# Kernel optimization log

Hardware: AMD Instinct MI355X
Metric: run time of the kernel (lower is better)

## Reference

```python
import jax, jax.numpy as jnp
import numpy as np

N = 40000      # nodes
E = 640000     # edges (avg degree 16)
F = 128        # num_features
D = 128        # embedding_size
G = 128        # graphs in batch


def _glorot(key, shape):
    fan_in = shape[-1]
    return jax.random.normal(key, shape, jnp.float32) / np.float32(np.sqrt(fan_in))


def setup_inputs() -> dict:
    key = jax.random.key(0)
    ks = jax.random.split(key, 20)
    inp = {
        "x": jax.random.normal(ks[0], (N, F), jnp.float32),
        "edge_index": jax.random.randint(ks[1], (2, E), 0, N, dtype=jnp.int32),
        "batch_index": jnp.sort(jax.random.randint(ks[2], (N,), 0, G, dtype=jnp.int32)),
    }
    dims = [(D, F), (D, D), (D, D), (D, D)]
    for i, (dout, din) in enumerate(dims):
        inp[f"Wroot{i}"] = _glorot(ks[3 + 3 * i], (dout, din))
        inp[f"Wrel{i}"] = _glorot(ks[4 + 3 * i], (dout, din))
        inp[f"b{i}"] = jnp.zeros((dout,), jnp.float32)
    inp["Wout"] = _glorot(ks[18], (1, D))
    inp["bout"] = jnp.zeros((1,), jnp.float32)
    return inp


def _graph_conv(h, src, dst, Wroot, Wrel, b, num_nodes):
    # PyG GraphConv (aggr='add'): out_i = W_root x_i + W_rel * sum_{j->i} x_j + b
    # Linear commutes with the sum, so aggregate first then one dense GEMM.
    agg = jax.ops.segment_sum(h[src], dst, num_segments=num_nodes)  # [N, din]
    return h @ Wroot.T + agg @ Wrel.T + b


def reference(x, edge_index, batch_index,
              Wroot0, Wrel0, b0, Wroot1, Wrel1, b1,
              Wroot2, Wrel2, b2, Wroot3, Wrel3, b3,
              Wout, bout):
    src, dst = edge_index[0], edge_index[1]
    n = x.shape[0]
    h = x.astype(jnp.float32)
    layers = [(Wroot0, Wrel0, b0), (Wroot1, Wrel1, b1),
              (Wroot2, Wrel2, b2), (Wroot3, Wrel3, b3)]
    for Wr, Wn, b in layers:
        h = jax.nn.gelu(_graph_conv(h, src, dst, Wr, Wn, b, n), approximate=False)
        # dropout p=0.5 -> identity at eval time
    # global mean pool over graphs (gap)
    sums = jax.ops.segment_sum(h, batch_index, num_segments=G)        # [G, D]
    counts = jax.ops.segment_sum(jnp.ones((n,), jnp.float32), batch_index, num_segments=G)
    pooled = sums / jnp.maximum(counts, 1.0)[:, None]
    return pooled @ Wout.T + bout  # [G, 1]
```

## Files before the change

kernel.cpp:

```cpp
#include <hip/hip_runtime.h>
#include <hip/hip_bf16.h>

typedef __bf16 bf16x8 __attribute__((ext_vector_type(8)));
typedef float  f32x4  __attribute__((ext_vector_type(4)));

__device__ __forceinline__ float blo(unsigned v) { return __uint_as_float(v << 16); }
__device__ __forceinline__ float bhi(unsigned v) { return __uint_as_float(v & 0xffff0000u); }
__device__ __forceinline__ unsigned short f2bf(float f) {
    unsigned u = __float_as_uint(f);
    u += 0x7fffu + ((u >> 16) & 1u);
    return (unsigned short)(u >> 16);
}
__device__ __forceinline__ float gelu_f(float x) {
    float t = 0.7978845608028654f * (x + 0.044715f * x * x * x);
    float e = __expf(2.0f * t);
    float th = 1.0f - 2.0f / (1.0f + e);
    return 0.5f * x * (1.0f + th);
}


__global__ void degree_kernel(const int* __restrict__ dst, int* __restrict__ deg, int E) {
    int e = blockIdx.x * blockDim.x + threadIdx.x;
    if (e < E) atomicAdd(&deg[dst[e]], 1);
}

__global__ void chunk_sum_kernel(const int* __restrict__ deg, int* __restrict__ bsum, int n) {
    int i = blockIdx.x * 1024 + threadIdx.x;
    int v = (i < n) ? deg[i] : 0;
#pragma unroll
    for (int m = 1; m < 64; m <<= 1) v += __shfl_xor(v, m, 64);
    __shared__ int ws[16];
    int wave = threadIdx.x >> 6, lane = threadIdx.x & 63;
    if (lane == 0) ws[wave] = v;
    __syncthreads();
    if (threadIdx.x == 0) {
        int s = 0;
#pragma unroll
        for (int k = 0; k < 16; ++k) s += ws[k];
        bsum[blockIdx.x] = s;
    }
}

__global__ void chunk_scan_kernel(const int* __restrict__ bsum, int* __restrict__ bbase,
                                  int nb, int* __restrict__ offsets, int n, int E) {
    int lane = threadIdx.x;
    int v = (lane < nb) ? bsum[lane] : 0;
    int s = v;
#pragma unroll
    for (int m = 1; m < 64; m <<= 1) {
        int t = __shfl_up(s, m, 64);
        if (lane >= m) s += t;
    }
    if (lane < nb) bbase[lane] = s - v;
    if (lane == 0) offsets[n] = E;
}

__global__ void scan_apply_kernel(const int* __restrict__ deg, const int* __restrict__ bbase,
                                  int* __restrict__ offsets, int* __restrict__ cursor, int n) {
    int i = blockIdx.x * 1024 + threadIdx.x;
    int lane = threadIdx.x & 63, wave = threadIdx.x >> 6;
    int v = (i < n) ? deg[i] : 0;
    int s = v;
#pragma unroll
    for (int m = 1; m < 64; m <<= 1) {
        int t = __shfl_up(s, m, 64);
        if (lane >= m) s += t;
    }
    __shared__ int ws[16];
    if (lane == 63) ws[wave] = s;
    __syncthreads();
    if (wave == 0 && lane < 16) {
        int wv = ws[lane];
        int ss = wv;
#pragma unroll
        for (int m = 1; m < 16; m <<= 1) {
            int t = __shfl_up(ss, m, 64);
            if (lane >= m) ss += t;
        }
        ws[lane] = ss - wv;
    }
    __syncthreads();
    int excl = (s - v) + ws[wave] + bbase[blockIdx.x];
    if (i < n) { offsets[i] = excl; cursor[i] = excl; }
}

__global__ void scatter_kernel(const int* __restrict__ src, const int* __restrict__ dst,
                               int* __restrict__ cursor, int* __restrict__ sorted_src, int E) {
    int e = blockIdx.x * blockDim.x + threadIdx.x;
    if (e < E) {
        int d = dst[e];
        int pos = atomicAdd(&cursor[d], 1);
        sorted_src[pos] = src[e];
    }
}

__global__ void bounds_kernel(const int* __restrict__ batch, int* __restrict__ gstart,
                              int N, int G) {
    int g = blockIdx.x * blockDim.x + threadIdx.x;
    if (g <= G) {
        int lo = 0, hi = N;
        while (lo < hi) {
            int mid = (lo + hi) >> 1;
            if (batch[mid] < g) lo = mid + 1; else hi = mid;
        }
        gstart[g] = lo;
    }
}

__global__ void cvt_kernel(const float4* __restrict__ in, ushort4* __restrict__ out, int n4) {
    int i = blockIdx.x * blockDim.x + threadIdx.x;
    if (i < n4) {
        float4 f = in[i];
        ushort4 o; o.x = f2bf(f.x); o.y = f2bf(f.y); o.z = f2bf(f.z); o.w = f2bf(f.w);
        out[i] = o;
    }
}

__global__ void build_wcat_all(const float* __restrict__ Wr0, const float* __restrict__ Wn0,
                               const float* __restrict__ Wr1, const float* __restrict__ Wn1,
                               const float* __restrict__ Wr2, const float* __restrict__ Wn2,
                               const float* __restrict__ Wr3, const float* __restrict__ Wn3,
                               __hip_bfloat16* __restrict__ wcat) {
    int idx = blockIdx.x * blockDim.x + threadIdx.x;
    if (idx >= 4 * 128 * 256) return;
    int l = idx >> 15;
    int j = (idx >> 8) & 127, k = idx & 255;
    const float* Wr = (l == 0) ? Wr0 : (l == 1) ? Wr1 : (l == 2) ? Wr2 : Wr3;
    const float* Wn = (l == 0) ? Wn0 : (l == 1) ? Wn1 : (l == 2) ? Wn2 : Wn3;
    float v = (k < 128) ? Wr[j * 128 + k] : Wn[j * 128 + (k - 128)];
    wcat[idx] = __float2bfloat16(v);
}

#define LDS_STRIDE 264
__global__ __launch_bounds__(512, 4)
void layer_kernel(const __hip_bfloat16* __restrict__ h,
                  const int* __restrict__ offsets,
                  const int* __restrict__ sorted_src,
                  const __hip_bfloat16* __restrict__ Wcat,
                  const float* __restrict__ bias,
                  __hip_bfloat16* __restrict__ out, int N) {
    __shared__ char lds[64 * LDS_STRIDE];
    int wave = threadIdx.x >> 6;
    int lane = threadIdx.x & 63;
    int row0 = blockIdx.x * 64;
    int half = lane >> 5, fl = lane & 31;
    const uint2* hu = (const uint2*)h;

#pragma unroll 1
    for (int i = 0; i < 8; ++i) {
        int lr = wave * 8 + i;
        int node = row0 + lr;
        if (node < N) {
            int s = offsets[node], e = offsets[node + 1];
            f32x4 A0 = {0,0,0,0}, A1 = {0,0,0,0}, A2 = {0,0,0,0}, A3 = {0,0,0,0};
            int t = s;
            for (; t + 8 <= e; t += 8) {
                int j0 = sorted_src[t + half];
                int j1 = sorted_src[t + 2 + half];
                int j2 = sorted_src[t + 4 + half];
                int j3 = sorted_src[t + 6 + half];
                uint2 v0 = hu[(size_t)j0 * 32 + fl];
                uint2 v1 = hu[(size_t)j1 * 32 + fl];
                uint2 v2 = hu[(size_t)j2 * 32 + fl];
                uint2 v3 = hu[(size_t)j3 * 32 + fl];
                A0[0] += blo(v0.x); A0[1] += bhi(v0.x); A0[2] += blo(v0.y); A0[3] += bhi(v0.y);
                A1[0] += blo(v1.x); A1[1] += bhi(v1.x); A1[2] += blo(v1.y); A1[3] += bhi(v1.y);
                A2[0] += blo(v2.x); A2[1] += bhi(v2.x); A2[2] += blo(v2.y); A2[3] += bhi(v2.y);
                A3[0] += blo(v3.x); A3[1] += bhi(v3.x); A3[2] += blo(v3.y); A3[3] += bhi(v3.y);
            }
            if (t + 4 <= e) {
                int j0 = sorted_src[t + half];
                int j1 = sorted_src[t + 2 + half];
                uint2 v0 = hu[(size_t)j0 * 32 + fl];
                uint2 v1 = hu[(size_t)j1 * 32 + fl];
                A0[0] += blo(v0.x); A0[1] += bhi(v0.x); A0[2] += blo(v0.y); A0[3] += bhi(v0.y);
                A1[0] += blo(v1.x); A1[1] += bhi(v1.x); A1[2] += blo(v1.y); A1[3] += bhi(v1.y);
                t += 4;
            }
            if (t + 2 <= e) {
                int j0 = sorted_src[t + half];
                uint2 v0 = hu[(size_t)j0 * 32 + fl];
                A0[0] += blo(v0.x); A0[1] += bhi(v0.x); A0[2] += blo(v0.y); A0[3] += bhi(v0.y);
                t += 2;
            }
            if (t < e && half == 0) {
                int j = sorted_src[t];
                uint2 v = hu[(size_t)j * 32 + fl];
                A1[0] += blo(v.x); A1[1] += bhi(v.x); A1[2] += blo(v.y); A1[3] += bhi(v.y);
            }
            float q0 = (A0[0] + A1[0]) + (A2[0] + A3[0]); q0 += __shfl_xor(q0, 32, 64);
            float q1 = (A0[1] + A1[1]) + (A2[1] + A3[1]); q1 += __shfl_xor(q1, 32, 64);
            float q2 = (A0[2] + A1[2]) + (A2[2] + A3[2]); q2 += __shfl_xor(q2, 32, 64);
            float q3 = (A0[3] + A1[3]) + (A2[3] + A3[3]); q3 += __shfl_xor(q3, 32, 64);
            if (half == 0) {
                ushort4 o; o.x = f2bf(q0); o.y = f2bf(q1); o.z = f2bf(q2); o.w = f2bf(q3);
                *reinterpret_cast<ushort4*>(&lds[lr * LDS_STRIDE + fl * 8]) = o;
            }
        }
    }
    __syncthreads();

    int la  = lane & 15;
    int keg = lane >> 4;
    int ke0 = keg * 8;
    int col = wave * 16 + la;

    bf16x8 b[8];
#pragma unroll
    for (int ks = 0; ks < 8; ++ks)
        b[ks] = *reinterpret_cast<const bf16x8*>(&Wcat[(size_t)col * 256 + ks * 32 + ke0]);
    float bv = bias[col];

    f32x4 acc[4];
#pragma unroll
    for (int m = 0; m < 4; ++m) {
        int r = row0 + m * 16 + la;
        if (r >= N) r = N - 1;
        const __hip_bfloat16* hr = &h[(size_t)r * 128];
        bf16x8 a[8];
#pragma unroll
        for (int ks = 0; ks < 4; ++ks)
            a[ks] = *reinterpret_cast<const bf16x8*>(&hr[ks * 32 + ke0]);
#pragma unroll
        for (int ks = 0; ks < 4; ++ks)
            a[ks + 4] = *reinterpret_cast<const bf16x8*>(
                &lds[(m * 16 + la) * LDS_STRIDE + ks * 64 + keg * 16]);
        f32x4 c = {0, 0, 0, 0};
#pragma unroll
        for (int ks = 0; ks < 8; ++ks)
            c = __builtin_amdgcn_mfma_f32_16x16x32_bf16(a[ks], b[ks], c, 0, 0, 0);
        acc[m] = c;
    }

    int r0 = row0 + (lane >> 4) * 4;
#pragma unroll
    for (int m = 0; m < 4; ++m) {
#pragma unroll
        for (int j = 0; j < 4; ++j) {
            int r = r0 + m * 16 + j;
            if (r < N)
                out[(size_t)r * 128 + col] = __float2bfloat16(gelu_f(acc[m][j] + bv));
        }
    }
}


__global__ void pool_partial(const __hip_bfloat16* __restrict__ h,
                             const int* __restrict__ batch,
                             const float* __restrict__ Wout,
                             float* __restrict__ outsum, int N) {
    int wid = blockIdx.x * 4 + (threadIdx.x >> 6);
    int lane = threadIdx.x & 63;
    int i0 = wid * 16;
    if (i0 >= N) return;
    int half = lane >> 5, fl = lane & 31;
    const uint2* hu = (const uint2*)h;
    float w0 = Wout[4 * fl], w1 = Wout[4 * fl + 1];
    float w2 = Wout[4 * fl + 2], w3 = Wout[4 * fl + 3];
    float dot = 0.f;
    int cur = -1;
#pragma unroll
    for (int t = 0; t < 8; ++t) {
        int i = i0 + 2 * t + half;
        if (i < N) {
            int g = batch[i];
            uint2 v = hu[(size_t)i * 32 + fl];
            float d = blo(v.x) * w0 + bhi(v.x) * w1 + blo(v.y) * w2 + bhi(v.y) * w3;
            if (g != cur) {
                if (cur >= 0) {
                    float r = dot;
#pragma unroll
                    for (int m = 16; m >= 1; m >>= 1) r += __shfl_xor(r, m, 64);
                    if (fl == 0) atomicAdd(&outsum[cur], r);
                }
                cur = g; dot = d;
            } else {
                dot += d;
            }
        }
    }
    if (cur >= 0) {
        float r = dot;
#pragma unroll
        for (int m = 16; m >= 1; m >>= 1) r += __shfl_xor(r, m, 64);
        if (fl == 0) atomicAdd(&outsum[cur], r);
    }
}

__global__ void pool_finish(const float* __restrict__ outsum,
                            const int* __restrict__ gstart,
                            const float* __restrict__ bout,
                            float* __restrict__ out, int G) {
    int g = blockIdx.x * blockDim.x + threadIdx.x;
    if (g < G) {
        float cnt = (float)(gstart[g + 1] - gstart[g]);
        out[g] = outsum[g] / fmaxf(cnt, 1.0f) + bout[0];
    }
}


extern "C" void kernel_launch(void* const* d_in, const int* in_sizes, int n_in,
                              void* d_out, int out_size, void* d_ws, size_t ws_size,
                              hipStream_t stream) {
    const float* x          = (const float*)d_in[0];
    const int*   edge_index = (const int*)d_in[1];
    const int*   batch      = (const int*)d_in[2];
    const float* Wroot[4] = {(const float*)d_in[3], (const float*)d_in[6],
                             (const float*)d_in[9], (const float*)d_in[12]};
    const float* Wrel[4]  = {(const float*)d_in[4], (const float*)d_in[7],
                             (const float*)d_in[10], (const float*)d_in[13]};
    const float* bias[4]  = {(const float*)d_in[5], (const float*)d_in[8],
                             (const float*)d_in[11], (const float*)d_in[14]};
    const float* Wout = (const float*)d_in[15];
    const float* bout = (const float*)d_in[16];
    float* out = (float*)d_out;

    const int N = in_sizes[2];
    const int E = in_sizes[1] / 2;
    const int G = 128;
    const int* src = edge_index;
    const int* dst = edge_index + E;

    char* ws = (char*)d_ws;
    size_t o = 0;
    auto alloc = [&](size_t bytes) { void* p = ws + o; o += (bytes + 255) & ~(size_t)255; return p; };

    __hip_bfloat16* hx   = (__hip_bfloat16*)alloc((size_t)N * 128 * 2);
    __hip_bfloat16* hb0  = (__hip_bfloat16*)alloc((size_t)N * 128 * 2);
    __hip_bfloat16* hb1  = (__hip_bfloat16*)alloc((size_t)N * 128 * 2);
    __hip_bfloat16* wcat = (__hip_bfloat16*)alloc((size_t)4 * 128 * 256 * 2);
    int* deg     = (int*)alloc((size_t)N * 4);
    int* offsets = (int*)alloc((size_t)(N + 1) * 4);
    int* cursor  = (int*)alloc((size_t)N * 4);
    int* sorted  = (int*)alloc((size_t)E * 4);
    int* gstart  = (int*)alloc((size_t)(G + 1) * 4);
    int* bsum    = (int*)alloc(64 * 4);
    int* bbase   = (int*)alloc(64 * 4);
    float* outsum = (float*)alloc((size_t)G * 4);

    const int nb = (N + 1023) / 1024;

    hipMemsetAsync(deg, 0, (size_t)N * 4, stream);
    degree_kernel<<<(E + 255) / 256, 256, 0, stream>>>(dst, deg, E);
    chunk_sum_kernel<<<nb, 1024, 0, stream>>>(deg, bsum, N);
    chunk_scan_kernel<<<1, 64, 0, stream>>>(bsum, bbase, nb, offsets, N, E);
    scan_apply_kernel<<<nb, 1024, 0, stream>>>(deg, bbase, offsets, cursor, N);
    scatter_kernel<<<(E + 255) / 256, 256, 0, stream>>>(src, dst, cursor, sorted, E);
    bounds_kernel<<<1, 256, 0, stream>>>(batch, gstart, N, G);

    cvt_kernel<<<(N * 128 / 4 + 255) / 256, 256, 0, stream>>>(
        (const float4*)x, (ushort4*)hx, N * 128 / 4);
    build_wcat_all<<<(4 * 128 * 256 + 255) / 256, 256, 0, stream>>>(
        Wroot[0], Wrel[0], Wroot[1], Wrel[1], Wroot[2], Wrel[2], Wroot[3], Wrel[3], wcat);

    __hip_bfloat16* hin = hx;
    __hip_bfloat16* houts[4] = {hb0, hb1, hb0, hb1};
    for (int l = 0; l < 4; ++l) {
        layer_kernel<<<(N + 63) / 64, 512, 0, stream>>>(
            hin, offsets, sorted, wcat + (size_t)l * 128 * 256, bias[l], houts[l], N);
        hin = houts[l];
    }

    hipMemsetAsync(outsum, 0, (size_t)G * 4, stream);
    pool_partial<<<((N + 15) / 16 + 3) / 4, 256, 0, stream>>>(hin, batch, Wout, outsum, N);
    pool_finish<<<1, 128, 0, stream>>>(outsum, gstart, bout, out, G);
}
```

Baseline: 399.4 us.

## Merge small setup and pooling kernels to cut launch count

```diff
diff --git a/kernel.cpp b/kernel.cpp
--- a/kernel.cpp
+++ b/kernel.cpp
@@ -19,9 +19,25 @@
 }
 
 
-__global__ void degree_kernel(const int* __restrict__ dst, int* __restrict__ deg, int E) {
+__global__ void degree_bounds_kernel(const int* __restrict__ dst, int* __restrict__ deg, int E,
+                                     const int* __restrict__ batch, int* __restrict__ gstart,
+                                     int N, int G, float* __restrict__ outsum,
+                                     int* __restrict__ done) {
     int e = blockIdx.x * blockDim.x + threadIdx.x;
     if (e < E) atomicAdd(&deg[dst[e]], 1);
+    if (blockIdx.x == 0) {
+        int t = threadIdx.x;
+        if (t <= G) {
+            int lo = 0, hi = N;
+            while (lo < hi) {
+                int mid = (lo + hi) >> 1;
+                if (batch[mid] < t) lo = mid + 1; else hi = mid;
+            }
+            gstart[t] = lo;
+        }
+        if (t < G) outsum[t] = 0.f;
+        if (t == 255) *done = 0;
+    }
 }
 
 __global__ void chunk_sum_kernel(const int* __restrict__ deg, int* __restrict__ bsum, int n) {
@@ -41,32 +57,31 @@
     }
 }
 
-__global__ void chunk_scan_kernel(const int* __restrict__ bsum, int* __restrict__ bbase,
-                                  int nb, int* __restrict__ offsets, int n, int E) {
-    int lane = threadIdx.x;
-    int v = (lane < nb) ? bsum[lane] : 0;
+__global__ void scan_apply_kernel(const int* __restrict__ deg, const int* __restrict__ bsum,
+                                  int nb, int* __restrict__ offsets, int* __restrict__ cursor,
+                                  int n, int E) {
+    __shared__ int base_s;
+    __shared__ int ws[16];
+    int lane = threadIdx.x & 63, wave = threadIdx.x >> 6;
+    if (wave == 0) {
+        int v = (lane < nb) ? bsum[lane] : 0;
+        int s = v;
+#pragma unroll
+        for (int m = 1; m < 64; m <<= 1) {
+            int t = __shfl_up(s, m, 64);
+            if (lane >= m) s += t;
+        }
+        if (lane == (int)blockIdx.x) base_s = s - v;
+    }
+    __syncthreads();
+    int i = blockIdx.x * 1024 + threadIdx.x;
+    int v = (i < n) ? deg[i] : 0;
     int s = v;
 #pragma unroll
     for (int m = 1; m < 64; m <<= 1) {
         int t = __shfl_up(s, m, 64);
         if (lane >= m) s += t;
     }
-    if (lane < nb) bbase[lane] = s - v;
-    if (lane == 0) offsets[n] = E;
-}
-
-__global__ void scan_apply_kernel(const int* __restrict__ deg, const int* __restrict__ bbase,
-                                  int* __restrict__ offsets, int* __restrict__ cursor, int n) {
-    int i = blockIdx.x * 1024 + threadIdx.x;
-    int lane = threadIdx.x & 63, wave = threadIdx.x >> 6;
-    int v = (i < n) ? deg[i] : 0;
-    int s = v;
-#pragma unroll
-    for (int m = 1; m < 64; m <<= 1) {
-        int t = __shfl_up(s, m, 64);
-        if (lane >= m) s += t;
-    }
-    __shared__ int ws[16];
     if (lane == 63) ws[wave] = s;
     __syncthreads();
     if (wave == 0 && lane < 16) {
@@ -80,8 +95,9 @@
         ws[lane] = ss - wv;
     }
     __syncthreads();
-    int excl = (s - v) + ws[wave] + bbase[blockIdx.x];
+    int excl = (s - v) + ws[wave] + base_s;
     if (i < n) { offsets[i] = excl; cursor[i] = excl; }
+    if (blockIdx.x == 0 && threadIdx.x == 0) offsets[n] = E;
 }
 
 __global__ void scatter_kernel(const int* __restrict__ src, const int* __restrict__ dst,
@@ -94,41 +110,26 @@
     }
 }
 
-__global__ void bounds_kernel(const int* __restrict__ batch, int* __restrict__ gstart,
-                              int N, int G) {
-    int g = blockIdx.x * blockDim.x + threadIdx.x;
-    if (g <= G) {
-        int lo = 0, hi = N;
-        while (lo < hi) {
-            int mid = (lo + hi) >> 1;
-            if (batch[mid] < g) lo = mid + 1; else hi = mid;
-        }
-        gstart[g] = lo;
-    }
-}
-
-__global__ void cvt_kernel(const float4* __restrict__ in, ushort4* __restrict__ out, int n4) {
+__global__ void prep_kernel(const float4* __restrict__ x4, ushort4* __restrict__ hx4, int n4,
+                            const float* __restrict__ Wr0, const float* __restrict__ Wn0,
+                            const float* __restrict__ Wr1, const float* __restrict__ Wn1,
+                            const float* __restrict__ Wr2, const float* __restrict__ Wn2,
+                            const float* __restrict__ Wr3, const float* __restrict__ Wn3,
+                            __hip_bfloat16* __restrict__ wcat) {
     int i = blockIdx.x * blockDim.x + threadIdx.x;
     if (i < n4) {
-        float4 f = in[i];
+        float4 f = x4[i];
         ushort4 o; o.x = f2bf(f.x); o.y = f2bf(f.y); o.z = f2bf(f.z); o.w = f2bf(f.w);
-        out[i] = o;
-    }
-}
-
-__global__ void build_wcat_all(const float* __restrict__ Wr0, const float* __restrict__ Wn0,
-                               const float* __restrict__ Wr1, const float* __restrict__ Wn1,
-                               const float* __restrict__ Wr2, const float* __restrict__ Wn2,
-                               const float* __restrict__ Wr3, const float* __restrict__ Wn3,
-                               __hip_bfloat16* __restrict__ wcat) {
-    int idx = blockIdx.x * blockDim.x + threadIdx.x;
-    if (idx >= 4 * 128 * 256) return;
-    int l = idx >> 15;
-    int j = (idx >> 8) & 127, k = idx & 255;
-    const float* Wr = (l == 0) ? Wr0 : (l == 1) ? Wr1 : (l == 2) ? Wr2 : Wr3;
-    const float* Wn = (l == 0) ? Wn0 : (l == 1) ? Wn1 : (l == 2) ? Wn2 : Wn3;
-    float v = (k < 128) ? Wr[j * 128 + k] : Wn[j * 128 + (k - 128)];
-    wcat[idx] = __float2bfloat16(v);
+        hx4[i] = o;
+    }
+    if (i < 4 * 128 * 256) {
+        int l = i >> 15;
+        int j = (i >> 8) & 127, k = i & 255;
+        const float* Wr = (l == 0) ? Wr0 : (l == 1) ? Wr1 : (l == 2) ? Wr2 : Wr3;
+        const float* Wn = (l == 0) ? Wn0 : (l == 1) ? Wn1 : (l == 2) ? Wn2 : Wn3;
+        float v = (k < 128) ? Wr[j * 128 + k] : Wn[j * 128 + (k - 128)];
+        wcat[i] = __float2bfloat16(v);
+    }
 }
 
 #define LDS_STRIDE 264
@@ -245,56 +246,62 @@
 }
 
 
-__global__ void pool_partial(const __hip_bfloat16* __restrict__ h,
-                             const int* __restrict__ batch,
-                             const float* __restrict__ Wout,
-                             float* __restrict__ outsum, int N) {
+__global__ void pool_kernel(const __hip_bfloat16* __restrict__ h,
+                            const int* __restrict__ batch,
+                            const float* __restrict__ Wout,
+                            const int* __restrict__ gstart,
+                            const float* __restrict__ bout,
+                            float* __restrict__ outsum, int* __restrict__ done,
+                            float* __restrict__ out, int N, int G, int nblocks) {
     int wid = blockIdx.x * 4 + (threadIdx.x >> 6);
     int lane = threadIdx.x & 63;
     int i0 = wid * 16;
-    if (i0 >= N) return;
     int half = lane >> 5, fl = lane & 31;
-    const uint2* hu = (const uint2*)h;
-    float w0 = Wout[4 * fl], w1 = Wout[4 * fl + 1];
-    float w2 = Wout[4 * fl + 2], w3 = Wout[4 * fl + 3];
-    float dot = 0.f;
-    int cur = -1;
-#pragma unroll
-    for (int t = 0; t < 8; ++t) {
-        int i = i0 + 2 * t + half;
-        if (i < N) {
-            int g = batch[i];
-            uint2 v = hu[(size_t)i * 32 + fl];
-            float d = blo(v.x) * w0 + bhi(v.x) * w1 + blo(v.y) * w2 + bhi(v.y) * w3;
-            if (g != cur) {
-                if (cur >= 0) {
-                    float r = dot;
-#pragma unroll
-                    for (int m = 16; m >= 1; m >>= 1) r += __shfl_xor(r, m, 64);
-                    if (fl == 0) atomicAdd(&outsum[cur], r);
+    if (i0 < N) {
+        const uint2* hu = (const uint2*)h;
+        float w0 = Wout[4 * fl], w1 = Wout[4 * fl + 1];
+        float w2 = Wout[4 * fl + 2], w3 = Wout[4 * fl + 3];
+        float dot = 0.f;
+        int cur = -1;
+#pragma unroll
+        for (int t = 0; t < 8; ++t) {
+            int i = i0 + 2 * t + half;
+            if (i < N) {
+                int g = batch[i];
+                uint2 v = hu[(size_t)i * 32 + fl];
+                float d = blo(v.x) * w0 + bhi(v.x) * w1 + blo(v.y) * w2 + bhi(v.y) * w3;
+                if (g != cur) {
+                    if (cur >= 0) {
+                        float r = dot;
+#pragma unroll
+                        for (int m = 16; m >= 1; m >>= 1) r += __shfl_xor(r, m, 64);
+                        if (fl == 0) atomicAdd(&outsum[cur], r);
+                    }
+                    cur = g; dot = d;
+                } else {
+                    dot += d;
                 }
-                cur = g; dot = d;
-            } else {
-                dot += d;
-            }
-        }
-    }
-    if (cur >= 0) {
-        float r = dot;
-#pragma unroll
-        for (int m = 16; m >= 1; m >>= 1) r += __shfl_xor(r, m, 64);
-        if (fl == 0) atomicAdd(&outsum[cur], r);
-    }
-}
-
-__global__ void pool_finish(const float* __restrict__ outsum,
-                            const int* __restrict__ gstart,
-                            const float* __restrict__ bout,
-                            float* __restrict__ out, int G) {
-    int g = blockIdx.x * blockDim.x + threadIdx.x;
-    if (g < G) {
-        float cnt = (float)(gstart[g + 1] - gstart[g]);
-        out[g] = outsum[g] / fmaxf(cnt, 1.0f) + bout[0];
+            }
+        }
+        if (cur >= 0) {
+            float r = dot;
+#pragma unroll
+            for (int m = 16; m >= 1; m >>= 1) r += __shfl_xor(r, m, 64);
+            if (fl == 0) atomicAdd(&outsum[cur], r);
+        }
+    }
+    __threadfence();
+    __syncthreads();
+    __shared__ int is_last;
+    if (threadIdx.x == 0) is_last = (atomicAdd(done, 1) == nblocks - 1);
+    __syncthreads();
+    if (is_last) {
+        __threadfence();
+        int t = threadIdx.x;
+        if (t < G) {
+            float cnt = (float)(gstart[t + 1] - gstart[t]);
+            out[t] = outsum[t] / fmaxf(cnt, 1.0f) + bout[0];
+        }
     }
 }
 
@@ -335,22 +342,20 @@
     int* sorted  = (int*)alloc((size_t)E * 4);
     int* gstart  = (int*)alloc((size_t)(G + 1) * 4);
     int* bsum    = (int*)alloc(64 * 4);
-    int* bbase   = (int*)alloc(64 * 4);
     float* outsum = (float*)alloc((size_t)G * 4);
+    int* done    = (int*)alloc(4);
 
     const int nb = (N + 1023) / 1024;
 
     hipMemsetAsync(deg, 0, (size_t)N * 4, stream);
-    degree_kernel<<<(E + 255) / 256, 256, 0, stream>>>(dst, deg, E);
+    degree_bounds_kernel<<<(E + 255) / 256, 256, 0, stream>>>(
+        dst, deg, E, batch, gstart, N, G, outsum, done);
     chunk_sum_kernel<<<nb, 1024, 0, stream>>>(deg, bsum, N);
-    chunk_scan_kernel<<<1, 64, 0, stream>>>(bsum, bbase, nb, offsets, N, E);
-    scan_apply_kernel<<<nb, 1024, 0, stream>>>(deg, bbase, offsets, cursor, N);
+    scan_apply_kernel<<<nb, 1024, 0, stream>>>(deg, bsum, nb, offsets, cursor, N, E);
     scatter_kernel<<<(E + 255) / 256, 256, 0, stream>>>(src, dst, cursor, sorted, E);
-    bounds_kernel<<<1, 256, 0, stream>>>(batch, gstart, N, G);
-
-    cvt_kernel<<<(N * 128 / 4 + 255) / 256, 256, 0, stream>>>(
-        (const float4*)x, (ushort4*)hx, N * 128 / 4);
-    build_wcat_all<<<(4 * 128 * 256 + 255) / 256, 256, 0, stream>>>(
+
+    prep_kernel<<<(N * 128 / 4 + 255) / 256, 256, 0, stream>>>(
+        (const float4*)x, (ushort4*)hx, N * 128 / 4,
         Wroot[0], Wrel[0], Wroot[1], Wrel[1], Wroot[2], Wrel[2], Wroot[3], Wrel[3], wcat);
 
     __hip_bfloat16* hin = hx;
@@ -361,7 +366,7 @@
         hin = houts[l];
     }
 
-    hipMemsetAsync(outsum, 0, (size_t)G * 4, stream);
-    pool_partial<<<((N + 15) / 16 + 3) / 4, 256, 0, stream>>>(hin, batch, Wout, outsum, N);
-    pool_finish<<<1, 128, 0, stream>>>(outsum, gstart, bout, out, G);
-}
+    int pool_blocks = ((N + 15) / 16 + 3) / 4;
+    pool_kernel<<<pool_blocks, 256, 0, stream>>>(
+        hin, batch, Wout, gstart, bout, outsum, done, out, N, G, pool_blocks);
+}
```

After: 416.1 us. 1.04x slower.
